# Performance work log

Hardware: AMD Instinct MI355X
Metric: run time of the kernel (lower is better)

## Reference

```python
import jax, jax.numpy as jnp
import numpy as np

BS = 64   # sparsity_block_size
B, R, C = 8, 64, 64


def setup_inputs() -> dict:
    key = jax.random.key(0)
    # causal block-lower-triangular layout: block (r,c) present iff c <= r
    tril = jnp.tril(jnp.ones((R, C), dtype=jnp.int32))
    sparsity_layout = jnp.broadcast_to(tril[None], (B, R, C)).astype(jnp.int32)
    n_sparse_blocks = B * (R * (R + 1) // 2)  # 16640
    x = jax.random.normal(key, (n_sparse_blocks, BS, BS), dtype=jnp.float32)
    return {"x": x, "sparsity_layout": sparsity_layout}


def reference(x, sparsity_layout):
    # x: [n_blocks, bs, bs]; sparsity_layout: [B, R, C] with sum == n_blocks.
    n, bs, _ = x.shape
    Bb, Rr, Cc = sparsity_layout.shape
    flat = sparsity_layout.reshape(-1)                       # [B*R*C]
    # reverse LUT: index into x for each present block (row-major nonzero order)
    rev = jnp.cumsum(flat) - 1                               # [B*R*C]
    present = (flat == 1)
    # to_dense (block form), fill -inf for absent blocks
    gathered = x[jnp.clip(rev, 0)]                           # [B*R*C, bs, bs]
    neg_inf = jnp.asarray(-jnp.inf, dtype=x.dtype)
    blocks = jnp.where(present[:, None, None], gathered, neg_inf)
    # arrange into dense rows: [B, R, bs, C*bs] (softmax over full dense last dim)
    rows = blocks.reshape(Bb, Rr, Cc, bs, bs).transpose(0, 1, 3, 2, 4).reshape(Bb, Rr, bs, Cc * bs)
    sm = jax.nn.softmax(rows, axis=-1)
    # back to block form
    sm_blocks = sm.reshape(Bb, Rr, bs, Cc, bs).transpose(0, 1, 3, 2, 4).reshape(Bb * Rr * Cc, bs, bs)
    # to_sparse: scatter present blocks back to their slots (absent -> dump slot n)
    idx = jnp.where(present, rev, n)
    out = jnp.zeros((n + 1, bs, bs), dtype=x.dtype).at[idx].set(sm_blocks)
    return out[:n]
```

## Files before the change

kernel.cpp:

```cpp
#include <hip/hip_runtime.h>
#include <math.h>


__global__ __launch_bounds__(256) void bs_softmax_kernel(
    const float* __restrict__ x, float* __restrict__ out) {
    const int w    = (blockIdx.x << 2) + (threadIdx.x >> 6);
    const int lane = threadIdx.x & 63;

    const int i = w & 63;
    const int r = 63 - ((w >> 6) & 63);
    const int b = w >> 12;

    const int base = (b * 2080 + ((r * (r + 1)) >> 1)) * 4096 + i * 64;
    const int nvec = (r + 1) << 4;

    const int j   = (lane << 2) & 63;
    const int cb0 = lane >> 4;
    const float* p0 = x + base + cb0 * 4096 + j;

    float4 v[16];
    float m = -INFINITY;

    #pragma unroll
    for (int k = 0; k < 16; ++k) {
        const int vi = lane + (k << 6);
        if (vi < nvec) {
            const float4 val = *(const float4*)(p0 + k * 16384);
            v[k] = val;
            m = fmaxf(m, fmaxf(fmaxf(val.x, val.y), fmaxf(val.z, val.w)));
        } else {
            v[k] = make_float4(-INFINITY, -INFINITY, -INFINITY, -INFINITY);
        }
    }

    #pragma unroll
    for (int off = 32; off >= 1; off >>= 1)
        m = fmaxf(m, __shfl_xor(m, off, 64));

    float s = 0.0f;
    #pragma unroll
    for (int k = 0; k < 16; ++k) {
        float4 val = v[k];
        val.x = __expf(val.x - m);
        val.y = __expf(val.y - m);
        val.z = __expf(val.z - m);
        val.w = __expf(val.w - m);
        v[k] = val;
        s += (val.x + val.y) + (val.z + val.w);
    }
    #pragma unroll
    for (int off = 32; off >= 1; off >>= 1)
        s += __shfl_xor(s, off, 64);
    const float inv = 1.0f / s;

    float* q0 = out + base + cb0 * 4096 + j;
    #pragma unroll
    for (int k = 0; k < 16; ++k) {
        const int vi = lane + (k << 6);
        if (vi < nvec) {
            float4 val = v[k];
            val.x *= inv; val.y *= inv; val.z *= inv; val.w *= inv;
            *(float4*)(q0 + k * 16384) = val;
        }
    }
}

extern "C" void kernel_launch(void* const* d_in, const int* in_sizes, int n_in,
                              void* d_out, int out_size, void* d_ws, size_t ws_size,
                              hipStream_t stream) {
    const float* x = (const float*)d_in[0];
    float* out = (float*)d_out;
    dim3 grid(8 * 64 * 64 / 4);
    dim3 block(256);
    bs_softmax_kernel<<<grid, block, 0, stream>>>(x, out);
}
```

Baseline: 436.4 us.

## Remap workgroups to four rows per block with cross-wave LDS reduction

```diff
diff --git a/kernel.cpp b/kernel.cpp
--- a/kernel.cpp
+++ b/kernel.cpp
@@ -4,28 +4,29 @@
 
 __global__ __launch_bounds__(256) void bs_softmax_kernel(
     const float* __restrict__ x, float* __restrict__ out) {
-    const int w    = (blockIdx.x << 2) + (threadIdx.x >> 6);
+    const int wg   = blockIdx.x;
+    const int i0   = wg & 15;
+    const int r    = 63 - ((wg >> 4) & 63);
+    const int b    = wg >> 10;
+
+    const int w    = threadIdx.x >> 6;
     const int lane = threadIdx.x & 63;
+    const int lr   = lane >> 4;
+    const int jj   = (lane & 15) << 2;
 
-    const int i = w & 63;
-    const int r = 63 - ((w >> 6) & 63);
-    const int b = w >> 12;
+    const int blk0 = b * 2080 + ((r * (r + 1)) >> 1);
+    const int off0 = blk0 * 4096 + (((i0 << 2) + lr) << 6) + jj;
+    const float* p0 = x + off0;
 
-    const int base = (b * 2080 + ((r * (r + 1)) >> 1)) * 4096 + i * 64;
-    const int nvec = (r + 1) << 4;
-
-    const int j   = (lane << 2) & 63;
-    const int cb0 = lane >> 4;
-    const float* p0 = x + base + cb0 * 4096 + j;
+    const int nb = (r >= w) ? (((r - w) >> 2) + 1) : 0;
 
     float4 v[16];
     float m = -INFINITY;
 
     #pragma unroll
     for (int k = 0; k < 16; ++k) {
-        const int vi = lane + (k << 6);
-        if (vi < nvec) {
-            const float4 val = *(const float4*)(p0 + k * 16384);
+        if (k < nb) {
+            const float4 val = *(const float4*)(p0 + ((w + (k << 2)) << 12));
             v[k] = val;
             m = fmaxf(m, fmaxf(fmaxf(val.x, val.y), fmaxf(val.z, val.w)));
         } else {
@@ -34,8 +35,14 @@
     }
 
     #pragma unroll
-    for (int off = 32; off >= 1; off >>= 1)
+    for (int off = 8; off >= 1; off >>= 1)
         m = fmaxf(m, __shfl_xor(m, off, 64));
+
+    __shared__ float redm[4][4];
+    __shared__ float reds[4][4];
+    if ((lane & 15) == 0) redm[w][lr] = m;
+    __syncthreads();
+    m = fmaxf(fmaxf(redm[0][lr], redm[1][lr]), fmaxf(redm[2][lr], redm[3][lr]));
 
     float s = 0.0f;
     #pragma unroll
@@ -49,18 +56,20 @@
         s += (val.x + val.y) + (val.z + val.w);
     }
     #pragma unroll
-    for (int off = 32; off >= 1; off >>= 1)
+    for (int off = 8; off >= 1; off >>= 1)
         s += __shfl_xor(s, off, 64);
+    if ((lane & 15) == 0) reds[w][lr] = s;
+    __syncthreads();
+    s = (reds[0][lr] + reds[1][lr]) + (reds[2][lr] + reds[3][lr]);
     const float inv = 1.0f / s;
 
-    float* q0 = out + base + cb0 * 4096 + j;
+    float* q0 = out + off0;
     #pragma unroll
     for (int k = 0; k < 16; ++k) {
-        const int vi = lane + (k << 6);
-        if (vi < nvec) {
+        if (k < nb) {
             float4 val = v[k];
             val.x *= inv; val.y *= inv; val.z *= inv; val.w *= inv;
-            *(float4*)(q0 + k * 16384) = val;
+            *(float4*)(q0 + ((w + (k << 2)) << 12)) = val;
         }
     }
 }
@@ -70,7 +79,7 @@
                               hipStream_t stream) {
     const float* x = (const float*)d_in[0];
     float* out = (float*)d_out;
-    dim3 grid(8 * 64 * 64 / 4);
+    dim3 grid(8 * 64 * 16);
     dim3 block(256);
     bs_softmax_kernel<<<grid, block, 0, stream>>>(x, out);
 }
```

Result: no change. 435.8 us (-0.1%).
